# Performance work log

Measured on AMD Instinct MI355X. Metric: run time of the kernel, lower is better.

Reference implementation:

```python
import jax, jax.numpy as jnp
import numpy as np

B, CIN, T = 64, 64, 4096
F, K = 128, 64


def setup_inputs() -> dict:
    key = jax.random.key(0)
    k1, k2, k3, k4, k5 = jax.random.split(key, 5)
    x = jax.random.normal(k1, (B, CIN, T), dtype=jnp.float32)
    conv_weights = jax.random.normal(k2, (F, K), dtype=jnp.float32) * 0.2
    spat_weights = jax.random.normal(k3, (F, CIN), dtype=jnp.float32) * 0.2
    weight = jax.random.normal(k4, (F,), dtype=jnp.float32)
    bias = jax.random.normal(k5, (F,), dtype=jnp.float32)
    return {"x": x, "conv_weights": conv_weights, "spat_weights": spat_weights,
            "weight": weight, "bias": bias}


def reference(x, conv_weights, spat_weights, weight, bias):
    n_filters, ksize = conv_weights.shape
    n_in = spat_weights.shape[1]
    # rank-1 merged kernel: [F, Cin, K]
    merged = conv_weights[:, None, :] * spat_weights[:, :, None]
    # valid conv1d: x [B,Cin,T] -> conved [B,F,T-K+1]
    conved = jax.lax.conv_general_dilated(
        x, merged, window_strides=(1,), padding='VALID',
        dimension_numbers=('NCH', 'OIH', 'NCH'))
    # per-filter weight norm
    norm_w = jnp.sqrt(jnp.sum(merged * merged, axis=(1, 2)))  # [F]
    # input norm: sliding-window sum of x^2 over channels and window
    sq = jnp.sum(x * x, axis=1, keepdims=True)  # [B,1,T]
    ones_k = jnp.ones((1, 1, ksize), dtype=x.dtype)
    slide = jax.lax.conv_general_dilated(
        sq, ones_k, window_strides=(1,), padding='VALID',
        dimension_numbers=('NCH', 'OIH', 'NCH'))[:, 0, :]  # [B,Tout]
    norm_inputs = jnp.sqrt(slide)
    scale = np.sqrt(n_in * ksize).astype(np.float32)
    cos_sims = conved / (norm_w[None, :, None] * norm_inputs[:, None, :]) * scale
    mean_cos = jnp.mean(jnp.abs(cos_sims), axis=2)  # [B,F]
    out_per_wave = mean_cos * weight[None, :] + bias[None, :]
    return jnp.sum(out_per_wave, axis=1)  # [B]
```

## Files before the change

### kernel.cpp

```cpp
#include <hip/hip_runtime.h>
#include <hip/hip_bf16.h>
#include <cstdint>
#include <cstddef>

#define BB   64
#define CINN 64
#define TS   4096
#define FF   128
#define KS   64
#define TOUT (TS - KS + 1)

#define TSEG 256
#define XROW 320
#define SXW  324
#define YWW  168
#define GF   32

typedef __attribute__((ext_vector_type(8))) short short8;
typedef __attribute__((ext_vector_type(4))) float f32x4;
union FragU { unsigned int u[4]; short8 v; uint4 q4; };

__device__ uint4 g_bandB[(size_t)FF * 3 * 64];
__device__ uint4 g_swF[(size_t)(FF / 16) * 2 * 64];
__device__ float g_wnf[FF];

static __device__ __forceinline__ unsigned int f2bf_u(float f) {
    __hip_bfloat16 h = __float2bfloat16(f);
    return (unsigned int)*reinterpret_cast<unsigned short*>(&h);
}

__global__ void k_band(const float* __restrict__ cw, const float* __restrict__ sw,
                       const float* __restrict__ weight) {
    const int f = blockIdx.x, l = threadIdx.x;
    const int n = l & 15, q = l >> 4;
    for (int s = 0; s < 3; ++s) {
        FragU o;
#pragma unroll
        for (int i = 0; i < 4; ++i) {
            int i0 = 32 * s + 8 * q + 2 * i - n;
            int i1 = i0 + 1;
            float a = (i0 >= 0 && i0 < KS) ? cw[(size_t)f * KS + i0] : 0.f;
            float c = (i1 >= 0 && i1 < KS) ? cw[(size_t)f * KS + i1] : 0.f;
            o.u[i] = f2bf_u(a) | (f2bf_u(c) << 16);
        }
        g_bandB[((size_t)f * 3 + s) * 64 + l] = o.q4;
    }
    if ((f & 15) == 0) {
        const int ft = f >> 4;
        for (int s = 0; s < 2; ++s) {
            FragU o;
#pragma unroll
            for (int i = 0; i < 4; ++i) {
                const float* sr = sw + (size_t)(16 * ft + n) * CINN + 32 * s + 8 * q + 2 * i;
                o.u[i] = f2bf_u(sr[0]) | (f2bf_u(sr[1]) << 16);
            }
            g_swF[((size_t)ft * 2 + s) * 64 + l] = o.q4;
        }
    }
    float a = sw[(size_t)f * CINN + l], c = cw[(size_t)f * KS + l];
    float v = a * a, u = c * c;
    for (int off = 32; off > 0; off >>= 1) {
        v += __shfl_down(v, off, 64);
        u += __shfl_down(u, off, 64);
    }
    if (l == 0) g_wnf[f] = weight[f] * rsqrtf(v * u) * (64.0f / (float)TOUT);
}

__global__ __launch_bounds__(512, 4) void k_fused(
    const float* __restrict__ x, const float* __restrict__ bias,
    float* __restrict__ out)
{
    __shared__ unsigned int xT[32 * SXW];
    __shared__ unsigned int yL[GF * YWW];
    __shared__ float sqA[XROW];
    __shared__ float rinvA[XROW];
    __shared__ float wred[8];

    const int tid = threadIdx.x;
    const int w = tid >> 6, l = tid & 63;
    const int m = l & 15, q = l >> 4;
    const int b = blockIdx.y;
    const int t0 = blockIdx.x * TSEG;

    {
        const float* xb = x + (size_t)b * CINN * TS;
        float* sqp = (float*)yL;
        float4 s4a = {0.f, 0.f, 0.f, 0.f}, s4b = {0.f, 0.f, 0.f, 0.f};
#pragma unroll
        for (int r = 0; r < 4; ++r) {
            const int cp = w + 8 * r;
            const float* x0 = xb + (size_t)(2 * cp) * TS;
            {
                int p = t0 + 4 * l; if (p > TS - 4) p = TS - 4;
                float4 v0 = *(const float4*)(x0 + p);
                float4 v1 = *(const float4*)(x0 + TS + p);
                s4a.x += v0.x * v0.x + v1.x * v1.x;
                s4a.y += v0.y * v0.y + v1.y * v1.y;
                s4a.z += v0.z * v0.z + v1.z * v1.z;
                s4a.w += v0.w * v0.w + v1.w * v1.w;
                FragU o;
                o.u[0] = f2bf_u(v0.x) | (f2bf_u(v1.x) << 16);
                o.u[1] = f2bf_u(v0.y) | (f2bf_u(v1.y) << 16);
                o.u[2] = f2bf_u(v0.z) | (f2bf_u(v1.z) << 16);
                o.u[3] = f2bf_u(v0.w) | (f2bf_u(v1.w) << 16);
                *(uint4*)&xT[cp * SXW + 4 * l] = o.q4;
            }
            if (l < 16) {
                int p = t0 + 256 + 4 * l; if (p > TS - 4) p = TS - 4;
                float4 v0 = *(const float4*)(x0 + p);
                float4 v1 = *(const float4*)(x0 + TS + p);
                s4b.x += v0.x * v0.x + v1.x * v1.x;
                s4b.y += v0.y * v0.y + v1.y * v1.y;
                s4b.z += v0.z * v0.z + v1.z * v1.z;
                s4b.w += v0.w * v0.w + v1.w * v1.w;
                FragU o;
                o.u[0] = f2bf_u(v0.x) | (f2bf_u(v1.x) << 16);
                o.u[1] = f2bf_u(v0.y) | (f2bf_u(v1.y) << 16);
                o.u[2] = f2bf_u(v0.z) | (f2bf_u(v1.z) << 16);
                o.u[3] = f2bf_u(v0.w) | (f2bf_u(v1.w) << 16);
                *(uint4*)&xT[cp * SXW + 256 + 4 * l] = o.q4;
            }
        }
        *(float4*)(sqp + w * XROW + 4 * l) = s4a;
        if (l < 16) *(float4*)(sqp + w * XROW + 256 + 4 * l) = s4b;
    }
    __syncthreads();

    if (tid < XROW) {
        const float* sqp = (const float*)yL;
        float s = 0.f;
#pragma unroll
        for (int i = 0; i < 8; ++i) s += sqp[i * XROW + tid];
        sqA[tid] = s;
    }
    __syncthreads();

    if (w == 7 && l < 32) {
        const int base = 8 * l;
        float s = 0.f, hd[8], tl[8];
#pragma unroll
        for (int k = 0; k < 64; ++k) {
            float v = sqA[base + k];
            if (k < 8) hd[k] = v;
            s += v;
        }
#pragma unroll
        for (int j = 0; j < 8; ++j) tl[j] = sqA[base + 64 + j];
#pragma unroll
        for (int j = 0; j < 8; ++j) {
            int tpos = t0 + base + j;
            rinvA[base + j] = (tpos < TOUT) ? rsqrtf(s) : 0.f;
            s += tl[j] - hd[j];
        }
    }

    float acc = 0.f;
    for (int g = 0; g < 4; ++g) {
        {
            FragU s0[2], s1[2];
#pragma unroll
            for (int ftl = 0; ftl < 2; ++ftl) {
                const int ft = 2 * g + ftl;
                s0[ftl].q4 = g_swF[((size_t)ft * 2 + 0) * 64 + l];
                s1[ftl].q4 = g_swF[((size_t)ft * 2 + 1) * 64 + l];
            }
            for (int tt = w; tt < 20; tt += 8) {
                FragU b0, b1;
#pragma unroll
                for (int i = 0; i < 4; ++i) {
                    b0.u[i] = xT[(4 * q + i) * SXW + 16 * tt + m];
                    b1.u[i] = xT[(16 + 4 * q + i) * SXW + 16 * tt + m];
                }
#pragma unroll
                for (int ftl = 0; ftl < 2; ++ftl) {
                    f32x4 d = {0.f, 0.f, 0.f, 0.f};
                    d = __builtin_amdgcn_mfma_f32_16x16x32_bf16(b0.v, s0[ftl].v, d, 0, 0, 0);
                    d = __builtin_amdgcn_mfma_f32_16x16x32_bf16(b1.v, s1[ftl].v, d, 0, 0, 0);
                    const int fl = 16 * ftl + m;
                    uint2 o;
                    o.x = f2bf_u(d[0]) | (f2bf_u(d[1]) << 16);
                    o.y = f2bf_u(d[2]) | (f2bf_u(d[3]) << 16);
                    *(uint2*)(yL + fl * YWW + 8 * tt + 2 * q) = o;
                }
            }
            if (g == 0 && tid < 256) yL[(tid >> 3) * YWW + 160 + (tid & 7)] = 0u;
        }
        __syncthreads();

        {
            float rr[4];
#pragma unroll
            for (int r = 0; r < 4; ++r) rr[r] = rinvA[64 * q + 16 * r + m];
#pragma unroll 2
            for (int j = 0; j < 4; ++j) {
                const int fl = 4 * w + j;
                const int f  = GF * g + fl;
                const uint4* bb = g_bandB + (size_t)f * 3 * 64;
                FragU B0, B1, B2;
                B0.q4 = bb[l]; B1.q4 = bb[64 + l]; B2.q4 = bb[128 + l];
                const int abase = fl * YWW + 8 * m + 4 * q;
                FragU a0, a1, a2;
                a0.q4 = *(const uint4*)(yL + abase);
                a1.q4 = *(const uint4*)(yL + abase + 16);
                a2.q4 = *(const uint4*)(yL + abase + 32);
                f32x4 d = {0.f, 0.f, 0.f, 0.f};
                d = __builtin_amdgcn_mfma_f32_16x16x32_bf16(a0.v, B0.v, d, 0, 0, 0);
                d = __builtin_amdgcn_mfma_f32_16x16x32_bf16(a1.v, B1.v, d, 0, 0, 0);
                d = __builtin_amdgcn_mfma_f32_16x16x32_bf16(a2.v, B2.v, d, 0, 0, 0);
                float facc = 0.f;
#pragma unroll
                for (int r = 0; r < 4; ++r) facc += fabsf(d[r]) * rr[r];
                acc += g_wnf[f] * facc;
            }
        }
        __syncthreads();
    }

    for (int off = 32; off > 0; off >>= 1) acc += __shfl_down(acc, off, 64);
    if (l == 0) wred[w] = acc;
    __syncthreads();
    if (tid == 0) {
        float s = 0.f;
#pragma unroll
        for (int i = 0; i < 8; ++i) s += wred[i];
        atomicAdd(out + b, s);
    }
    if (blockIdx.x == 0 && tid < FF) {
        float v = bias[tid];
        for (int off = 32; off > 0; off >>= 1) v += __shfl_down(v, off, 64);
        if ((tid & 63) == 0) atomicAdd(out + b, v);
    }
}

extern "C" void kernel_launch(void* const* d_in, const int* in_sizes, int n_in,
                              void* d_out, int out_size, void* d_ws, size_t ws_size,
                              hipStream_t stream) {
    const float* x  = (const float*)d_in[0];
    const float* cw = (const float*)d_in[1];
    const float* sw = (const float*)d_in[2];
    const float* w  = (const float*)d_in[3];
    const float* bs = (const float*)d_in[4];
    float* out = (float*)d_out;

    (void)d_ws; (void)ws_size;

    hipMemsetAsync(d_out, 0, (size_t)out_size * sizeof(float), stream);
    k_band <<<dim3(FF), 64, 0, stream>>>(cw, sw, w);
    k_fused<<<dim3(TS / TSEG, BB), 512, 0, stream>>>(x, bs, out);
}
```

Before: 128.9 us.

## Process two time tiles per block with register prefetch of next tile

Each block now handles two consecutive 256-sample time segments, which halves the grid. The main part of the second segment's x data is prefetched into registers while the first segment's MFMA work runs, so global load latency overlaps compute. The cost is more register pressure from the prefetch buffer, fewer blocks to spread across CUs, and a serialised two-tile loop per block.

```diff
diff --git a/kernel.cpp b/kernel.cpp
--- a/kernel.cpp
+++ b/kernel.cpp
@@ -80,20 +80,35 @@
     const int w = tid >> 6, l = tid & 63;
     const int m = l & 15, q = l >> 4;
     const int b = blockIdx.y;
-    const int t0 = blockIdx.x * TSEG;
-
-    {
-        const float* xb = x + (size_t)b * CINN * TS;
-        float* sqp = (float*)yL;
-        float4 s4a = {0.f, 0.f, 0.f, 0.f}, s4b = {0.f, 0.f, 0.f, 0.f};
+    const int gx = blockIdx.x;
+
+    const float* xb = x + (size_t)b * CINN * TS;
+
+    float4 xa[4][2];
+    auto loadx = [&](int tb) {
 #pragma unroll
         for (int r = 0; r < 4; ++r) {
             const int cp = w + 8 * r;
             const float* x0 = xb + (size_t)(2 * cp) * TS;
-            {
-                int p = t0 + 4 * l; if (p > TS - 4) p = TS - 4;
-                float4 v0 = *(const float4*)(x0 + p);
-                float4 v1 = *(const float4*)(x0 + TS + p);
+            int p = tb + 4 * l; if (p > TS - 4) p = TS - 4;
+            xa[r][0] = *(const float4*)(x0 + p);
+            xa[r][1] = *(const float4*)(x0 + TS + p);
+        }
+    };
+    loadx(2 * gx * TSEG);
+
+    float acc = 0.f;
+
+    for (int tile = 0; tile < 2; ++tile) {
+        const int t0 = (2 * gx + tile) * TSEG;
+
+        {
+            float* sqp = (float*)yL;
+            float4 s4a = {0.f, 0.f, 0.f, 0.f}, s4b = {0.f, 0.f, 0.f, 0.f};
+#pragma unroll
+            for (int r = 0; r < 4; ++r) {
+                const int cp = w + 8 * r;
+                float4 v0 = xa[r][0], v1 = xa[r][1];
                 s4a.x += v0.x * v0.x + v1.x * v1.x;
                 s4a.y += v0.y * v0.y + v1.y * v1.y;
                 s4a.z += v0.z * v0.z + v1.z * v1.z;
@@ -106,114 +121,120 @@
                 *(uint4*)&xT[cp * SXW + 4 * l] = o.q4;
             }
             if (l < 16) {
-                int p = t0 + 256 + 4 * l; if (p > TS - 4) p = TS - 4;
-                float4 v0 = *(const float4*)(x0 + p);
-                float4 v1 = *(const float4*)(x0 + TS + p);
-                s4b.x += v0.x * v0.x + v1.x * v1.x;
-                s4b.y += v0.y * v0.y + v1.y * v1.y;
-                s4b.z += v0.z * v0.z + v1.z * v1.z;
-                s4b.w += v0.w * v0.w + v1.w * v1.w;
-                FragU o;
-                o.u[0] = f2bf_u(v0.x) | (f2bf_u(v1.x) << 16);
-                o.u[1] = f2bf_u(v0.y) | (f2bf_u(v1.y) << 16);
-                o.u[2] = f2bf_u(v0.z) | (f2bf_u(v1.z) << 16);
-                o.u[3] = f2bf_u(v0.w) | (f2bf_u(v1.w) << 16);
-                *(uint4*)&xT[cp * SXW + 256 + 4 * l] = o.q4;
-            }
-        }
-        *(float4*)(sqp + w * XROW + 4 * l) = s4a;
-        if (l < 16) *(float4*)(sqp + w * XROW + 256 + 4 * l) = s4b;
-    }
-    __syncthreads();
-
-    if (tid < XROW) {
-        const float* sqp = (const float*)yL;
-        float s = 0.f;
-#pragma unroll
-        for (int i = 0; i < 8; ++i) s += sqp[i * XROW + tid];
-        sqA[tid] = s;
-    }
-    __syncthreads();
-
-    if (w == 7 && l < 32) {
-        const int base = 8 * l;
-        float s = 0.f, hd[8], tl[8];
-#pragma unroll
-        for (int k = 0; k < 64; ++k) {
-            float v = sqA[base + k];
-            if (k < 8) hd[k] = v;
-            s += v;
-        }
-#pragma unroll
-        for (int j = 0; j < 8; ++j) tl[j] = sqA[base + 64 + j];
-#pragma unroll
-        for (int j = 0; j < 8; ++j) {
-            int tpos = t0 + base + j;
-            rinvA[base + j] = (tpos < TOUT) ? rsqrtf(s) : 0.f;
-            s += tl[j] - hd[j];
-        }
-    }
-
-    float acc = 0.f;
-    for (int g = 0; g < 4; ++g) {
-        {
-            FragU s0[2], s1[2];
-#pragma unroll
-            for (int ftl = 0; ftl < 2; ++ftl) {
-                const int ft = 2 * g + ftl;
-                s0[ftl].q4 = g_swF[((size_t)ft * 2 + 0) * 64 + l];
-                s1[ftl].q4 = g_swF[((size_t)ft * 2 + 1) * 64 + l];
-            }
-            for (int tt = w; tt < 20; tt += 8) {
-                FragU b0, b1;
-#pragma unroll
-                for (int i = 0; i < 4; ++i) {
-                    b0.u[i] = xT[(4 * q + i) * SXW + 16 * tt + m];
-                    b1.u[i] = xT[(16 + 4 * q + i) * SXW + 16 * tt + m];
-                }
+#pragma unroll
+                for (int r = 0; r < 4; ++r) {
+                    const int cp = w + 8 * r;
+                    const float* x0 = xb + (size_t)(2 * cp) * TS;
+                    int p = t0 + 256 + 4 * l; if (p > TS - 4) p = TS - 4;
+                    float4 v0 = *(const float4*)(x0 + p);
+                    float4 v1 = *(const float4*)(x0 + TS + p);
+                    s4b.x += v0.x * v0.x + v1.x * v1.x;
+                    s4b.y += v0.y * v0.y + v1.y * v1.y;
+                    s4b.z += v0.z * v0.z + v1.z * v1.z;
+                    s4b.w += v0.w * v0.w + v1.w * v1.w;
+                    FragU o;
+                    o.u[0] = f2bf_u(v0.x) | (f2bf_u(v1.x) << 16);
+                    o.u[1] = f2bf_u(v0.y) | (f2bf_u(v1.y) << 16);
+                    o.u[2] = f2bf_u(v0.z) | (f2bf_u(v1.z) << 16);
+                    o.u[3] = f2bf_u(v0.w) | (f2bf_u(v1.w) << 16);
+                    *(uint4*)&xT[cp * SXW + 256 + 4 * l] = o.q4;
+                }
+            }
+            *(float4*)(sqp + w * XROW + 4 * l) = s4a;
+            if (l < 16) *(float4*)(sqp + w * XROW + 256 + 4 * l) = s4b;
+        }
+        __syncthreads();
+
+        if (tile == 0) loadx((2 * gx + 1) * TSEG);
+
+        if (tid < XROW) {
+            const float* sqp = (const float*)yL;
+            float s = 0.f;
+#pragma unroll
+            for (int i = 0; i < 8; ++i) s += sqp[i * XROW + tid];
+            sqA[tid] = s;
+        }
+        __syncthreads();
+
+        if (w == 7 && l < 32) {
+            const int base = 8 * l;
+            float s = 0.f, hd[8], tl[8];
+#pragma unroll
+            for (int k = 0; k < 64; ++k) {
+                float v = sqA[base + k];
+                if (k < 8) hd[k] = v;
+                s += v;
+            }
+#pragma unroll
+            for (int j = 0; j < 8; ++j) tl[j] = sqA[base + 64 + j];
+#pragma unroll
+            for (int j = 0; j < 8; ++j) {
+                int tpos = t0 + base + j;
+                rinvA[base + j] = (tpos < TOUT) ? rsqrtf(s) : 0.f;
+                s += tl[j] - hd[j];
+            }
+        }
+
+        for (int g = 0; g < 4; ++g) {
+            {
+                FragU s0[2], s1[2];
 #pragma unroll
                 for (int ftl = 0; ftl < 2; ++ftl) {
+                    const int ft = 2 * g + ftl;
+                    s0[ftl].q4 = g_swF[((size_t)ft * 2 + 0) * 64 + l];
+                    s1[ftl].q4 = g_swF[((size_t)ft * 2 + 1) * 64 + l];
+                }
+                for (int tt = w; tt < 20; tt += 8) {
+                    FragU b0, b1;
+#pragma unroll
+                    for (int i = 0; i < 4; ++i) {
+                        b0.u[i] = xT[(4 * q + i) * SXW + 16 * tt + m];
+                        b1.u[i] = xT[(16 + 4 * q + i) * SXW + 16 * tt + m];
+                    }
+#pragma unroll
+                    for (int ftl = 0; ftl < 2; ++ftl) {
+                        f32x4 d = {0.f, 0.f, 0.f, 0.f};
+                        d = __builtin_amdgcn_mfma_f32_16x16x32_bf16(b0.v, s0[ftl].v, d, 0, 0, 0);
+                        d = __builtin_amdgcn_mfma_f32_16x16x32_bf16(b1.v, s1[ftl].v, d, 0, 0, 0);
+                        const int fl = 16 * ftl + m;
+                        uint2 o;
+                        o.x = f2bf_u(d[0]) | (f2bf_u(d[1]) << 16);
+                        o.y = f2bf_u(d[2]) | (f2bf_u(d[3]) << 16);
+                        *(uint2*)(yL + fl * YWW + 8 * tt + 2 * q) = o;
+                    }
+                }
+                if (g == 0 && tid < 256) yL[(tid >> 3) * YWW + 160 + (tid & 7)] = 0u;
+            }
+            __syncthreads();
+
+            {
+                float rr[4];
+#pragma unroll
+                for (int r = 0; r < 4; ++r) rr[r] = rinvA[64 * q + 16 * r + m];
+#pragma unroll 2
+                for (int j = 0; j < 4; ++j) {
+                    const int fl = 4 * w + j;
+                    const int f  = GF * g + fl;
+                    const uint4* bb = g_bandB + (size_t)f * 3 * 64;
+                    FragU B0, B1, B2;
+                    B0.q4 = bb[l]; B1.q4 = bb[64 + l]; B2.q4 = bb[128 + l];
+                    const int abase = fl * YWW + 8 * m + 4 * q;
+                    FragU a0, a1, a2;
+                    a0.q4 = *(const uint4*)(yL + abase);
+                    a1.q4 = *(const uint4*)(yL + abase + 16);
+                    a2.q4 = *(const uint4*)(yL + abase + 32);
                     f32x4 d = {0.f, 0.f, 0.f, 0.f};
-                    d = __builtin_amdgcn_mfma_f32_16x16x32_bf16(b0.v, s0[ftl].v, d, 0, 0, 0);
-                    d = __builtin_amdgcn_mfma_f32_16x16x32_bf16(b1.v, s1[ftl].v, d, 0, 0, 0);
-                    const int fl = 16 * ftl + m;
-                    uint2 o;
-                    o.x = f2bf_u(d[0]) | (f2bf_u(d[1]) << 16);
-                    o.y = f2bf_u(d[2]) | (f2bf_u(d[3]) << 16);
-                    *(uint2*)(yL + fl * YWW + 8 * tt + 2 * q) = o;
-                }
-            }
-            if (g == 0 && tid < 256) yL[(tid >> 3) * YWW + 160 + (tid & 7)] = 0u;
-        }
-        __syncthreads();
-
-        {
-            float rr[4];
-#pragma unroll
-            for (int r = 0; r < 4; ++r) rr[r] = rinvA[64 * q + 16 * r + m];
-#pragma unroll 2
-            for (int j = 0; j < 4; ++j) {
-                const int fl = 4 * w + j;
-                const int f  = GF * g + fl;
-                const uint4* bb = g_bandB + (size_t)f * 3 * 64;
-                FragU B0, B1, B2;
-                B0.q4 = bb[l]; B1.q4 = bb[64 + l]; B2.q4 = bb[128 + l];
-                const int abase = fl * YWW + 8 * m + 4 * q;
-                FragU a0, a1, a2;
-                a0.q4 = *(const uint4*)(yL + abase);
-                a1.q4 = *(const uint4*)(yL + abase + 16);
-                a2.q4 = *(const uint4*)(yL + abase + 32);
-                f32x4 d = {0.f, 0.f, 0.f, 0.f};
-                d = __builtin_amdgcn_mfma_f32_16x16x32_bf16(a0.v, B0.v, d, 0, 0, 0);
-                d = __builtin_amdgcn_mfma_f32_16x16x32_bf16(a1.v, B1.v, d, 0, 0, 0);
-                d = __builtin_amdgcn_mfma_f32_16x16x32_bf16(a2.v, B2.v, d, 0, 0, 0);
-                float facc = 0.f;
-#pragma unroll
-                for (int r = 0; r < 4; ++r) facc += fabsf(d[r]) * rr[r];
-                acc += g_wnf[f] * facc;
-            }
-        }
-        __syncthreads();
+                    d = __builtin_amdgcn_mfma_f32_16x16x32_bf16(a0.v, B0.v, d, 0, 0, 0);
+                    d = __builtin_amdgcn_mfma_f32_16x16x32_bf16(a1.v, B1.v, d, 0, 0, 0);
+                    d = __builtin_amdgcn_mfma_f32_16x16x32_bf16(a2.v, B2.v, d, 0, 0, 0);
+                    float facc = 0.f;
+#pragma unroll
+                    for (int r = 0; r < 4; ++r) facc += fabsf(d[r]) * rr[r];
+                    acc += g_wnf[f] * facc;
+                }
+            }
+            __syncthreads();
+        }
     }
 
     for (int off = 32; off > 0; off >>= 1) acc += __shfl_down(acc, off, 64);
@@ -225,7 +246,7 @@
         for (int i = 0; i < 8; ++i) s += wred[i];
         atomicAdd(out + b, s);
     }
-    if (blockIdx.x == 0 && tid < FF) {
+    if (gx == 0 && tid < FF) {
         float v = bias[tid];
         for (int off = 32; off > 0; off >>= 1) v += __shfl_down(v, off, 64);
         if ((tid & 63) == 0) atomicAdd(out + b, v);
@@ -246,5 +267,5 @@
 
     hipMemsetAsync(d_out, 0, (size_t)out_size * sizeof(float), stream);
     k_band <<<dim3(FF), 64, 0, stream>>>(cw, sw, w);
-    k_fused<<<dim3(TS / TSEG, BB), 512, 0, stream>>>(x, bs, out);
-}
+    k_fused<<<dim3(TS / TSEG / 2, BB), 512, 0, stream>>>(x, bs, out);
+}
```

Result: slower. 133.4 us (+3.5%).
